# Kernel optimization log

Measured on AMD Instinct MI355X. Metric: run time of the kernel, lower is better.

The kernel has to match this reference:

```python
import jax, jax.numpy as jnp
import numpy as np
from jax import lax

L, H, NUM_CONVS, KSIZE = 8192, 128, 4, 7
EPS = 1e-5


def _pos_encoding(length, dim, dtype):
    pos = jnp.arange(length, dtype=jnp.float32)[:, None]
    i = jnp.arange(dim, dtype=jnp.float32)[None, :]
    angle = pos / jnp.power(10000.0, (2.0 * jnp.floor(i / 2.0)) / dim)
    pe = jnp.where((jnp.arange(dim) % 2 == 0)[None, :], jnp.sin(angle), jnp.cos(angle))
    return pe.astype(dtype)


def _layer_norm(x):
    mu = jnp.mean(x, axis=-1, keepdims=True)
    var = jnp.mean(jnp.square(x - mu), axis=-1, keepdims=True)
    return (x - mu) * lax.rsqrt(var + EPS)


def _conv1d_same(x, w, b):
    # x: [L, H]; w: [H_out, H_in, K]; b: [H_out]. SAME padding over sequence.
    lhs = x.T[None]  # [1, H, L]
    out = lax.conv_general_dilated(lhs, w, window_strides=(1,), padding='SAME',
                                   dimension_numbers=('NCH', 'OIH', 'NCH'))
    return (out[0] + b[:, None]).T  # [L, H]


def setup_inputs() -> dict:
    key = jax.random.key(0)
    ks = jax.random.split(key, 12)
    s = 0.02
    return {
        'x': jax.random.normal(ks[0], (L, H), jnp.float32),
        'conv_w': jax.random.normal(ks[1], (NUM_CONVS, H, H, KSIZE), jnp.float32) * s,
        'conv_b': jax.random.normal(ks[2], (NUM_CONVS, H), jnp.float32) * s,
        'Wq': jax.random.normal(ks[3], (H, H), jnp.float32) * s,
        'bq': jax.random.normal(ks[4], (H,), jnp.float32) * s,
        'Wk': jax.random.normal(ks[5], (H, H), jnp.float32) * s,
        'bk': jax.random.normal(ks[6], (H,), jnp.float32) * s,
        'Wv': jax.random.normal(ks[7], (H, H), jnp.float32) * s,
        'bv': jax.random.normal(ks[8], (H,), jnp.float32) * s,
        'Wff': jax.random.normal(ks[9], (H, H), jnp.float32) * s,
        'bff': jax.random.normal(ks[10], (H,), jnp.float32) * s,
    }


def reference(x, conv_w, conv_b, Wq, bq, Wk, bk, Wv, bv, Wff, bff):
    h = x + _pos_encoding(x.shape[0], x.shape[1], x.dtype)
    # conv stack: LN -> conv -> residual, repeated num_convs times
    for i in range(NUM_CONVS):
        residual = h
        h = _conv1d_same(_layer_norm(h), conv_w[i], conv_b[i]) + residual
    # self-attention (single-head as written in the source)
    residual = h
    n = _layer_norm(h)
    q = n @ Wq.T + bq
    k = n @ Wk.T + bk
    v = n @ Wv.T + bv
    scale = 1.0 / jnp.sqrt(jnp.asarray(H, h.dtype))
    attn = jax.nn.softmax((q @ k.T) * scale, axis=-1)  # [L, L]
    h = attn @ v + residual
    # feed-forward
    residual = h
    h = jax.nn.relu(_layer_norm(h) @ Wff.T + bff) + residual
    return h
```

## Files before the change

### kernel.cpp

```cpp
#include <hip/hip_runtime.h>

#define LL 8192
#define HH 128

typedef __attribute__((ext_vector_type(8))) short short8v;
typedef __attribute__((ext_vector_type(4))) short short4v;
typedef __attribute__((ext_vector_type(4))) float f32x4;
typedef __attribute__((ext_vector_type(16))) float f32x16;

__device__ inline short f2bf(float f) {
    union { float f; unsigned u; } x; x.f = f;
    unsigned r = (x.u + 0x7fffu + ((x.u >> 16) & 1u)) >> 16;
    return (short)r;
}
__device__ inline float bf2f(short s) {
    union { unsigned u; float f; } x; x.u = ((unsigned)(unsigned short)s) << 16;
    return x.f;
}

__device__ inline void plane32swap(unsigned& a, unsigned& b) {
#if defined(__has_builtin)
#if __has_builtin(__builtin_amdgcn_permlane32_swap)
    typedef unsigned u2v __attribute__((ext_vector_type(2)));
    u2v r = __builtin_amdgcn_permlane32_swap(a, b, false, false);
    a = r[0]; b = r[1];
    return;
#endif
#endif
    asm volatile("v_permlane32_swap_b32 %0, %1" : "+v"(a), "+v"(b));
}

__device__ inline short* sAp(short* base, int row, int col) {
    int byte = (row << 8) + (col << 1);
    byte ^= (row & 7) << 4;
    return (short*)((char*)base + byte);
}

__device__ inline short8v ln_pack8(const float* rowF, int l15) {
    const float4 a = *(const float4*)&rowF[l15 * 8];
    const float4 b = *(const float4*)&rowF[l15 * 8 + 4];
    float s  = (a.x + a.y) + (a.z + a.w) + (b.x + b.y) + (b.z + b.w);
    float s2 = a.x * a.x + a.y * a.y + a.z * a.z + a.w * a.w
             + b.x * b.x + b.y * b.y + b.z * b.z + b.w * b.w;
#pragma unroll
    for (int off = 1; off <= 8; off <<= 1) {
        s  += __shfl_xor(s,  off, 64);
        s2 += __shfl_xor(s2, off, 64);
    }
    float mu = s * (1.f / 128.f);
    float var = s2 * (1.f / 128.f) - mu * mu;
    float rstd = rsqrtf(var + 1e-5f);
    short8v r;
    r[0] = f2bf((a.x - mu) * rstd);
    r[1] = f2bf((a.y - mu) * rstd);
    r[2] = f2bf((a.z - mu) * rstd);
    r[3] = f2bf((a.w - mu) * rstd);
    r[4] = f2bf((b.x - mu) * rstd);
    r[5] = f2bf((b.y - mu) * rstd);
    r[6] = f2bf((b.z - mu) * rstd);
    r[7] = f2bf((b.w - mu) * rstd);
    return r;
}

__global__ __launch_bounds__(256) void repack_all(const float* __restrict__ x,
                                                  const float* __restrict__ w,
                                                  const float* __restrict__ Wq,
                                                  const float* __restrict__ Wk,
                                                  const float* __restrict__ Wv,
                                                  const float* __restrict__ bq,
                                                  const float* __restrict__ bk,
                                                  const float* __restrict__ bv,
                                                  const float* __restrict__ Wff,
                                                  short* __restrict__ wkb,
                                                  short* __restrict__ wqkvb,
                                                  float* __restrict__ b3,
                                                  short* __restrict__ wffb,
                                                  float* __restrict__ h0) {
    const float qs = 0.08838834764831845f;
    int idx = blockIdx.x * 256 + threadIdx.x;
    if (idx < 458752) {
        int k = idx % 7;
        int t = idx / 7;
        int i = t % HH; t /= HH;
        int o = t % HH;
        int lay = t / HH;
        wkb[((lay * 7 + k) * HH + o) * HH + i] = f2bf(w[idx]);
    } else {
        int j = idx - 458752;
        if (j < 49152) {
            int t = j >> 14, r = j & 16383;
            float v = (t == 0) ? Wq[r] * qs : (t == 1) ? Wk[r] : Wv[r];
            wqkvb[j] = f2bf(v);
        } else if (j < 49536) {
            int jj = j - 49152;
            b3[jj] = (jj < 128) ? bq[jj] * qs : (jj < 256) ? bk[jj - 128] : bv[jj - 256];
        } else if (j < 65920) {
            int jj = j - 49536;
            wffb[jj] = f2bf(Wff[jj]);
        } else {
            int p = j - 65920;
            if (p < 262144) {
                int g = p >> 5, c4 = (p & 31) << 2;
                float4 val = *(const float4*)&x[g * HH + c4];
                float fg = (float)g;
#pragma unroll
                for (int h = 0; h < 2; h++) {
                    int i0 = c4 + h * 2;
                    float e = (float)i0 / 128.f;
                    float ang = fg / powf(10000.f, e);
                    ((float*)&val)[h * 2]     += sinf(ang);
                    ((float*)&val)[h * 2 + 1] += cosf(ang);
                }
                *(float4*)&h0[g * HH + c4] = val;
            }
        }
    }
}

__global__ __launch_bounds__(256, 4) void conv_layer_kernel(const float* __restrict__ hin,
                                                            const short* __restrict__ wkb,
                                                            const float* __restrict__ conv_b,
                                                            float* __restrict__ hout,
                                                            int lay) {
    __shared__ float sF[22][132];
    __shared__ short sA[22 * 128];
    int tid = threadIdx.x;
    int w = tid >> 6, lane = tid & 63;
    int l15 = lane & 15, quad = lane >> 4;
    int m0 = (blockIdx.x >> 1) * 16;
    int c0w = (blockIdx.x & 1) * 64 + w * 16;

    for (int idx = tid; idx < 22 * 32; idx += 256) {
        int r = idx >> 5, c4 = (idx & 31) << 2;
        int g = m0 - 3 + r;
        float4 val = make_float4(0.f, 0.f, 0.f, 0.f);
        if (g >= 0 && g < LL) val = *(const float4*)&hin[g * HH + c4];
        *(float4*)&sF[r][c4] = val;
    }
    __syncthreads();
#pragma unroll
    for (int rr = 0; rr < 2; rr++) {
        int row = rr * 16 + w * 4 + quad;
        if (row < 22)
            *(short8v*)sAp(sA, row, l15 * 8) = ln_pack8(&sF[row][0], l15);
    }
    __syncthreads();
    f32x4 accA = (f32x4)(0.f), accB = (f32x4)(0.f);
    const short* wl = wkb + lay * 7 * HH * HH;
    for (int k = 0; k < 7; k++) {
        const short* b0 = wl + (k * HH + c0w + l15) * HH;
#pragma unroll
        for (int ks = 0; ks < 4; ks++) {
            short8v bf = *(const short8v*)&b0[ks * 32 + quad * 8];
            short8v af = *(const short8v*)sAp(sA, l15 + k, ks * 32 + quad * 8);
            if (ks & 1) accB = __builtin_amdgcn_mfma_f32_16x16x32_bf16(af, bf, accB, 0, 0, 0);
            else        accA = __builtin_amdgcn_mfma_f32_16x16x32_bf16(af, bf, accA, 0, 0, 0);
        }
    }
    float bb = conv_b[lay * HH + c0w + l15];
#pragma unroll
    for (int r = 0; r < 4; r++) {
        int row = quad * 4 + r;
        hout[(m0 + row) * HH + c0w + l15] =
            sF[3 + row][c0w + l15] + accA[r] + accB[r] + bb;
    }
}

__global__ __launch_bounds__(256, 2) void conv_qkv_kernel(const float* __restrict__ hin,
                                                          const short* __restrict__ wkb,
                                                          const float* __restrict__ conv_b,
                                                          const short* __restrict__ wqkvb,
                                                          const float* __restrict__ b3,
                                                          float* __restrict__ hB,
                                                          short* __restrict__ qb,
                                                          short* __restrict__ kb,
                                                          short* __restrict__ vt) {
    __shared__ float sF[22][132];
    __shared__ short sA[22 * 128];
    __shared__ short sT[4][32][17];
    int tid = threadIdx.x;
    int w = tid >> 6, lane = tid & 63;
    int l15 = lane & 15, quad = lane >> 4;
    int m0 = blockIdx.x * 16;
    int c0 = w * 32;

    for (int idx = tid; idx < 22 * 32; idx += 256) {
        int r = idx >> 5, c4 = (idx & 31) << 2;
        int g = m0 - 3 + r;
        float4 val = make_float4(0.f, 0.f, 0.f, 0.f);
        if (g >= 0 && g < LL) val = *(const float4*)&hin[g * HH + c4];
        *(float4*)&sF[r][c4] = val;
    }
    __syncthreads();
#pragma unroll
    for (int rr = 0; rr < 2; rr++) {
        int row = rr * 16 + w * 4 + quad;
        if (row < 22)
            *(short8v*)sAp(sA, row, l15 * 8) = ln_pack8(&sF[row][0], l15);
    }
    __syncthreads();
    f32x4 a0 = (f32x4)(0.f), a1 = (f32x4)(0.f);
    const short* wl = wkb + 3 * 7 * HH * HH;
    for (int k = 0; k < 7; k++) {
        const short* b0 = wl + (k * HH + c0 + l15) * HH;
        const short* b1 = b0 + 16 * HH;
#pragma unroll
        for (int ks = 0; ks < 4; ks++) {
            short8v bf0 = *(const short8v*)&b0[ks * 32 + quad * 8];
            short8v bf1 = *(const short8v*)&b1[ks * 32 + quad * 8];
            short8v af = *(const short8v*)sAp(sA, l15 + k, ks * 32 + quad * 8);
            a0 = __builtin_amdgcn_mfma_f32_16x16x32_bf16(af, bf0, a0, 0, 0, 0);
            a1 = __builtin_amdgcn_mfma_f32_16x16x32_bf16(af, bf1, a1, 0, 0, 0);
        }
    }
    float bb0 = conv_b[3 * HH + c0 + l15], bb1 = conv_b[3 * HH + c0 + 16 + l15];
#pragma unroll
    for (int r = 0; r < 4; r++) {
        int row = quad * 4 + r;
        float v0 = sF[3 + row][c0 + l15]      + a0[r] + bb0;
        float v1 = sF[3 + row][c0 + 16 + l15] + a1[r] + bb1;
        sF[3 + row][c0 + l15]      = v0;
        sF[3 + row][c0 + 16 + l15] = v1;
        hB[(m0 + row) * HH + c0 + l15]      = v0;
        hB[(m0 + row) * HH + c0 + 16 + l15] = v1;
    }
    __syncthreads();
    {
        int row = w * 4 + quad;
        *(short8v*)sAp(sA, row, l15 * 8) = ln_pack8(&sF[3 + row][0], l15);
    }
    __syncthreads();
    short8v af4[4];
#pragma unroll
    for (int ks = 0; ks < 4; ks++)
        af4[ks] = *(const short8v*)sAp(sA, l15, ks * 32 + quad * 8);

    for (int t = 0; t < 3; t++) {
        f32x4 acc0 = (f32x4)(0.f), acc1 = (f32x4)(0.f);
        const short* b0 = wqkvb + (t * 128 + c0 + l15) * HH;
        const short* b1 = b0 + 16 * HH;
#pragma unroll
        for (int ks = 0; ks < 4; ks++) {
            short8v bf0 = *(const short8v*)&b0[ks * 32 + quad * 8];
            short8v bf1 = *(const short8v*)&b1[ks * 32 + quad * 8];
            acc0 = __builtin_amdgcn_mfma_f32_16x16x32_bf16(af4[ks], bf0, acc0, 0, 0, 0);
            acc1 = __builtin_amdgcn_mfma_f32_16x16x32_bf16(af4[ks], bf1, acc1, 0, 0, 0);
        }
        float qb0 = b3[t * 128 + c0 + l15], qb1 = b3[t * 128 + c0 + 16 + l15];
        if (t < 2) {
            short* o = (t == 0) ? qb : kb;
#pragma unroll
            for (int r = 0; r < 4; r++) {
                int lr = m0 + quad * 4 + r;
                o[lr * HH + c0 + l15]      = f2bf(acc0[r] + qb0);
                o[lr * HH + c0 + 16 + l15] = f2bf(acc1[r] + qb1);
            }
        } else {
#pragma unroll
            for (int r = 0; r < 4; r++) {
                sT[w][l15][quad * 4 + r]      = f2bf(acc0[r] + qb0);
                sT[w][16 + l15][quad * 4 + r] = f2bf(acc1[r] + qb1);
            }
            asm volatile("s_waitcnt lgkmcnt(0)" ::: "memory");
#pragma unroll
            for (int cc = 0; cc < 8; cc++) {
                int col = cc * 4 + quad;
                vt[(c0 + col) * LL + m0 + l15] = sT[w][col][l15];
            }
        }
    }
}

#define FBN 64

__global__ __launch_bounds__(256, 2) void flash_mfma_kernel(const short* __restrict__ qs,
                                                            const short* __restrict__ ksrc,
                                                            const short* __restrict__ vsrc,
                                                            short* __restrict__ PO,
                                                            float* __restrict__ Pl,
                                                            int segrows) {
    __shared__ short sK[2 * 16 * 64 * 8];
    __shared__ short sV[2 * 16 * 64 * 8];

    const int tid = threadIdx.x;
    const int w = tid >> 6, lane = tid & 63;
    const int l31 = lane & 31, hi = lane >> 5;
    const int m0 = blockIdx.x * 128;
    const int seg = blockIdx.y;
    const int jbeg = seg * segrows;
    const int nchunk = segrows >> 6;
    const int qrow = m0 + w * 32 + l31;

    short8v qf[8];
#pragma unroll
    for (int ks = 0; ks < 8; ks++)
        qf[ks] = *(const short8v*)&qs[qrow * HH + ks * 16 + hi * 8];

    float l_r = 0.f;
    f32x16 o_acc[4];
#pragma unroll
    for (int dt = 0; dt < 4; dt++) o_acc[dt] = (f32x16)(0.f);

    short8v kr[4], vr[4];
#pragma unroll
    for (int r = 0; r < 4; r++) {
        int s = w + 4 * r;
        kr[r] = *(const short8v*)&ksrc[(jbeg + (s >> 3) * 32 + l31) * HH + (s & 7) * 16 + hi * 8];
        vr[r] = *(const short8v*)&vsrc[((s >> 2) * 32 + l31) * LL + jbeg + (s & 3) * 16 + hi * 8];
    }
#pragma unroll
    for (int r = 0; r < 4; r++) {
        int s = w + 4 * r;
        *(short8v*)&sK[(s * 64 + lane) * 8] = kr[r];
        *(short8v*)&sV[(s * 64 + lane) * 8] = vr[r];
    }
    if (nchunk > 1) {
        const int j1 = jbeg + FBN;
#pragma unroll
        for (int r = 0; r < 4; r++) {
            int s = w + 4 * r;
            kr[r] = *(const short8v*)&ksrc[(j1 + (s >> 3) * 32 + l31) * HH + (s & 7) * 16 + hi * 8];
            vr[r] = *(const short8v*)&vsrc[((s >> 2) * 32 + l31) * LL + j1 + (s & 3) * 16 + hi * 8];
        }
    }
    __syncthreads();

    int cur = 0;
    for (int c = 0; c < nchunk; c++) {
        const int kb_ = cur * 8192;
        f32x16 s0 = (f32x16)(0.f), s1 = (f32x16)(0.f);
#pragma unroll
        for (int ks = 0; ks < 8; ks++) {
            short8v kf0 = *(const short8v*)&sK[kb_ + ((ks) * 64 + lane) * 8];
            short8v kf1 = *(const short8v*)&sK[kb_ + ((8 + ks) * 64 + lane) * 8];
            s0 = __builtin_amdgcn_mfma_f32_32x32x16_bf16(kf0, qf[ks], s0, 0, 0, 0);
            s1 = __builtin_amdgcn_mfma_f32_32x32x16_bf16(kf1, qf[ks], s1, 0, 0, 0);
        }
        if (c + 1 < nchunk) {
            const int nb = (cur ^ 1) * 8192;
#pragma unroll
            for (int r = 0; r < 4; r++) {
                int s = w + 4 * r;
                *(short8v*)&sK[nb + (s * 64 + lane) * 8] = kr[r];
                *(short8v*)&sV[nb + (s * 64 + lane) * 8] = vr[r];
            }
            if (c + 2 < nchunk) {
                const int j2 = jbeg + (c + 2) * FBN;
#pragma unroll
                for (int r = 0; r < 4; r++) {
                    int s = w + 4 * r;
                    kr[r] = *(const short8v*)&ksrc[(j2 + (s >> 3) * 32 + l31) * HH + (s & 7) * 16 + hi * 8];
                    vr[r] = *(const short8v*)&vsrc[((s >> 2) * 32 + l31) * LL + j2 + (s & 3) * 16 + hi * 8];
                }
            }
        }
        short8v pfrag[4];
#pragma unroll
        for (int nt = 0; nt < 2; nt++) {
            const f32x16& sa = nt ? s1 : s0;
            unsigned pw[8];
#pragma unroll
            for (int m = 0; m < 8; m++) {
                float p0 = __expf(fminf(sa[2 * m], 30.f));
                float p1 = __expf(fminf(sa[2 * m + 1], 30.f));
                l_r += p0 + p1;
                union { float f; unsigned u; } u0, u1;
                u0.f = p0; u1.f = p1;
                pw[m] = (u0.u >> 16) | (u1.u & 0xffff0000u);
            }
            plane32swap(pw[0], pw[2]);
            plane32swap(pw[1], pw[3]);
            plane32swap(pw[4], pw[6]);
            plane32swap(pw[5], pw[7]);
            union { unsigned u[4]; short8v v; } fa, fb;
            fa.u[0] = pw[0]; fa.u[1] = pw[1]; fa.u[2] = pw[2]; fa.u[3] = pw[3];
            fb.u[0] = pw[4]; fb.u[1] = pw[5]; fb.u[2] = pw[6]; fb.u[3] = pw[7];
            pfrag[nt * 2]     = fa.v;
            pfrag[nt * 2 + 1] = fb.v;
        }
#pragma unroll
        for (int ks = 0; ks < 4; ks++)
#pragma unroll
            for (int dt = 0; dt < 4; dt++) {
                short8v vf = *(const short8v*)&sV[kb_ + ((dt * 4 + ks) * 64 + lane) * 8];
                o_acc[dt] = __builtin_amdgcn_mfma_f32_32x32x16_bf16(pfrag[ks], vf, o_acc[dt], 0, 0, 0);
            }
        __syncthreads();
        cur ^= 1;
    }
    float lsum = l_r + __shfl_xor(l_r, 32, 64);
    if (hi == 0)
        Pl[seg * LL + qrow] = lsum;
#pragma unroll
    for (int dt = 0; dt < 4; dt++)
#pragma unroll
        for (int i = 0; i < 16; i++) {
            int qr = (i & 3) + 8 * (i >> 2) + 4 * hi;
            PO[(size_t)seg * LL * HH + (size_t)(m0 + w * 32 + qr) * HH + dt * 32 + l31] =
                f2bf(o_acc[dt][i]);
        }
}

__global__ __launch_bounds__(256) void ff_kernel(const float* __restrict__ hin,
                                                 const short* __restrict__ PO,
                                                 const float* __restrict__ Pl,
                                                 const short* __restrict__ wffb,
                                                 const float* __restrict__ bff,
                                                 float* __restrict__ out,
                                                 int nsplit) {
    __shared__ float sF[16][132];
    __shared__ short sA[16 * 128];
    __shared__ float sLi[16];
    int tid = threadIdx.x;
    int w = tid >> 6, lane = tid & 63;
    int l15 = lane & 15, quad = lane >> 4;
    int m0 = blockIdx.x * 16;

    if (tid < 16) {
        float s = 0.f;
        for (int seg = 0; seg < nsplit; seg++) s += Pl[seg * LL + m0 + tid];
        sLi[tid] = 1.f / s;
    }
    __syncthreads();
    for (int idx = tid; idx < 16 * 32; idx += 256) {
        int r = idx >> 5, c4 = (idx & 31) << 2;
        float4 hv = *(const float4*)&hin[(m0 + r) * HH + c4];
        float s0 = 0.f, s1 = 0.f, s2 = 0.f, s3 = 0.f;
        for (int seg = 0; seg < nsplit; seg++) {
            short4v pv = *(const short4v*)&PO[(size_t)seg * LL * HH + (m0 + r) * HH + c4];
            s0 += bf2f(pv[0]); s1 += bf2f(pv[1]); s2 += bf2f(pv[2]); s3 += bf2f(pv[3]);
        }
        float li = sLi[r];
        *(float4*)&sF[r][c4] = make_float4(hv.x + s0 * li, hv.y + s1 * li,
                                           hv.z + s2 * li, hv.w + s3 * li);
    }
    __syncthreads();
    {
        int row = w * 4 + quad;
        *(short8v*)sAp(sA, row, l15 * 8) = ln_pack8(&sF[row][0], l15);
    }
    __syncthreads();
    int c0 = w * 32;
    f32x4 acc0 = (f32x4)(0.f), acc1 = (f32x4)(0.f);
    const short* b0 = wffb + (c0 + l15) * HH;
    const short* b1 = b0 + 16 * HH;
#pragma unroll
    for (int ks = 0; ks < 4; ks++) {
        short8v af = *(const short8v*)sAp(sA, l15, ks * 32 + quad * 8);
        short8v bf0 = *(const short8v*)&b0[ks * 32 + quad * 8];
        short8v bf1 = *(const short8v*)&b1[ks * 32 + quad * 8];
        acc0 = __builtin_amdgcn_mfma_f32_16x16x32_bf16(af, bf0, acc0, 0, 0, 0);
        acc1 = __builtin_amdgcn_mfma_f32_16x16x32_bf16(af, bf1, acc1, 0, 0, 0);
    }
    float bb0 = bff[c0 + l15], bb1 = bff[c0 + 16 + l15];
#pragma unroll
    for (int r = 0; r < 4; r++) {
        int lr = quad * 4 + r;
        out[(m0 + lr) * HH + c0 + l15]      = fmaxf(acc0[r] + bb0, 0.f) + sF[lr][c0 + l15];
        out[(m0 + lr) * HH + c0 + 16 + l15] = fmaxf(acc1[r] + bb1, 0.f) + sF[lr][c0 + 16 + l15];
    }
}

extern "C" void kernel_launch(void* const* d_in, const int* in_sizes, int n_in,
                              void* d_out, int out_size, void* d_ws, size_t ws_size,
                              hipStream_t stream) {
    const float* x      = (const float*)d_in[0];
    const float* conv_w = (const float*)d_in[1];
    const float* conv_b = (const float*)d_in[2];
    const float* Wq = (const float*)d_in[3];
    const float* bq = (const float*)d_in[4];
    const float* Wk = (const float*)d_in[5];
    const float* bk = (const float*)d_in[6];
    const float* Wv = (const float*)d_in[7];
    const float* bv = (const float*)d_in[8];
    const float* Wff = (const float*)d_in[9];
    const float* bff = (const float*)d_in[10];
    float* out = (float*)d_out;

    char* ws = (char*)d_ws;
    const size_t MB = 1u << 20;
    float* hB   = (float*)(ws);
    short* qb   = (short*)(ws + 4 * MB);
    short* kb   = (short*)(ws + 6 * MB);
    short* vt   = (short*)(ws + 8 * MB);
    float* Pl   = (float*)(ws + 10 * MB);
    short* wffb = (short*)(ws + 10 * MB + 524288);
    short* PO   = (short*)(ws + 10 * MB + 524288 + 32768);
    short* wkb   = (short*)(ws + 16 * MB);
    short* wqkvb = (short*)(ws + 17 * MB);
    float* b3    = (float*)(ws + 17 * MB + 131072);
    float* h0    = (float*)(ws + 18 * MB);
    float* h13   = (float*)(ws + 22 * MB);
    float* h2    = h0;

    const int nsplit = 8;
    const int segrows = LL / nsplit;

    repack_all<<<3074, 256, 0, stream>>>(x, conv_w, Wq, Wk, Wv, bq, bk, bv, Wff,
                                         wkb, wqkvb, b3, wffb, h0);
    conv_layer_kernel<<<LL / 16 * 2, 256, 0, stream>>>(h0,  wkb, conv_b, h13, 0);
    conv_layer_kernel<<<LL / 16 * 2, 256, 0, stream>>>(h13, wkb, conv_b, h2,  1);
    conv_layer_kernel<<<LL / 16 * 2, 256, 0, stream>>>(h2,  wkb, conv_b, h13, 2);
    conv_qkv_kernel<<<LL / 16, 256, 0, stream>>>(h13, wkb, conv_b, wqkvb, b3,
                                                 hB, qb, kb, vt);
    flash_mfma_kernel<<<dim3(LL / 128, nsplit), 256, 0, stream>>>(qb, kb, vt, PO, Pl, segrows);
    ff_kernel<<<LL / 16, 256, 0, stream>>>(hB, PO, Pl, wffb, bff, out, nsplit);
}
```

Measured before the change: 211.6 us.

## Single-buffer flash LDS, exp2 softmax, setprio, and XCD-aware block remapping

The flash kernel goes from double-buffered to single-buffered LDS for K/V, using register prefetch with two barriers per chunk. It also wraps the MFMA phases in s_setprio. Softmax now uses a native exp2 with log2e folded into the Q scale, and drops the clamp at 30. P packing uses a perm instruction. Block indices in the conv, qkv, flash and ff kernels are remapped so neighbouring tiles land on the same XCD for L2 locality. The exp clamp removal could overflow for large logits, and the extra barrier reduces overlap.

```diff
diff --git a/kernel.cpp b/kernel.cpp
--- a/kernel.cpp
+++ b/kernel.cpp
@@ -16,6 +16,27 @@
 __device__ inline float bf2f(short s) {
     union { unsigned u; float f; } x; x.u = ((unsigned)(unsigned short)s) << 16;
     return x.f;
+}
+
+__device__ inline float fexp2(float x) {
+#if defined(__has_builtin)
+#if __has_builtin(__builtin_amdgcn_exp2f)
+    return __builtin_amdgcn_exp2f(x);
+#else
+    return __expf(x * 0.6931471805599453f);
+#endif
+#else
+    return __expf(x * 0.6931471805599453f);
+#endif
+}
+
+__device__ inline unsigned pack_hi16(unsigned hi, unsigned lo) {
+#if defined(__has_builtin)
+#if __has_builtin(__builtin_amdgcn_perm)
+    return __builtin_amdgcn_perm(hi, lo, 0x07060302u);
+#endif
+#endif
+    return (lo >> 16) | (hi & 0xffff0000u);
 }
 
 __device__ inline void plane32swap(unsigned& a, unsigned& b) {
@@ -76,7 +97,7 @@
                                                   float* __restrict__ b3,
                                                   short* __restrict__ wffb,
                                                   float* __restrict__ h0) {
-    const float qs = 0.08838834764831845f;
+    const float qs = 0.08838834764831845f * 1.4426950408889634f;
     int idx = blockIdx.x * 256 + threadIdx.x;
     if (idx < 458752) {
         int k = idx % 7;
@@ -127,8 +148,9 @@
     int tid = threadIdx.x;
     int w = tid >> 6, lane = tid & 63;
     int l15 = lane & 15, quad = lane >> 4;
-    int m0 = (blockIdx.x >> 1) * 16;
-    int c0w = (blockIdx.x & 1) * 64 + w * 16;
+    int wg = blockIdx.x;
+    int m0 = ((wg & 7) * 64 + (wg >> 4)) * 16;
+    int c0w = (((wg >> 3) & 1)) * 64 + w * 16;
 
     for (int idx = tid; idx < 22 * 32; idx += 256) {
         int r = idx >> 5, c4 = (idx & 31) << 2;
@@ -181,7 +203,8 @@
     int tid = threadIdx.x;
     int w = tid >> 6, lane = tid & 63;
     int l15 = lane & 15, quad = lane >> 4;
-    int m0 = blockIdx.x * 16;
+    int wg = blockIdx.x;
+    int m0 = ((wg & 7) * 64 + (wg >> 3)) * 16;
     int c0 = w * 32;
 
     for (int idx = tid; idx < 22 * 32; idx += 256) {
@@ -279,14 +302,14 @@
                                                             short* __restrict__ PO,
                                                             float* __restrict__ Pl,
                                                             int segrows) {
-    __shared__ short sK[2 * 16 * 64 * 8];
-    __shared__ short sV[2 * 16 * 64 * 8];
+    __shared__ short sK[16 * 64 * 8];
+    __shared__ short sV[16 * 64 * 8];
 
     const int tid = threadIdx.x;
     const int w = tid >> 6, lane = tid & 63;
     const int l31 = lane & 31, hi = lane >> 5;
-    const int m0 = blockIdx.x * 128;
-    const int seg = blockIdx.y;
+    const int seg = blockIdx.x & 7;
+    const int m0 = (blockIdx.x >> 3) * 128;
     const int jbeg = seg * segrows;
     const int nchunk = segrows >> 6;
     const int qrow = m0 + w * 32 + l31;
@@ -308,52 +331,35 @@
         kr[r] = *(const short8v*)&ksrc[(jbeg + (s >> 3) * 32 + l31) * HH + (s & 7) * 16 + hi * 8];
         vr[r] = *(const short8v*)&vsrc[((s >> 2) * 32 + l31) * LL + jbeg + (s & 3) * 16 + hi * 8];
     }
-#pragma unroll
-    for (int r = 0; r < 4; r++) {
-        int s = w + 4 * r;
-        *(short8v*)&sK[(s * 64 + lane) * 8] = kr[r];
-        *(short8v*)&sV[(s * 64 + lane) * 8] = vr[r];
-    }
-    if (nchunk > 1) {
-        const int j1 = jbeg + FBN;
+
+    for (int c = 0; c < nchunk; c++) {
+        __syncthreads();
 #pragma unroll
         for (int r = 0; r < 4; r++) {
             int s = w + 4 * r;
-            kr[r] = *(const short8v*)&ksrc[(j1 + (s >> 3) * 32 + l31) * HH + (s & 7) * 16 + hi * 8];
-            vr[r] = *(const short8v*)&vsrc[((s >> 2) * 32 + l31) * LL + j1 + (s & 3) * 16 + hi * 8];
-        }
-    }
-    __syncthreads();
-
-    int cur = 0;
-    for (int c = 0; c < nchunk; c++) {
-        const int kb_ = cur * 8192;
+            *(short8v*)&sK[(s * 64 + lane) * 8] = kr[r];
+            *(short8v*)&sV[(s * 64 + lane) * 8] = vr[r];
+        }
+        __syncthreads();
+        if (c + 1 < nchunk) {
+            const int j1 = jbeg + (c + 1) * FBN;
+#pragma unroll
+            for (int r = 0; r < 4; r++) {
+                int s = w + 4 * r;
+                kr[r] = *(const short8v*)&ksrc[(j1 + (s >> 3) * 32 + l31) * HH + (s & 7) * 16 + hi * 8];
+                vr[r] = *(const short8v*)&vsrc[((s >> 2) * 32 + l31) * LL + j1 + (s & 3) * 16 + hi * 8];
+            }
+        }
         f32x16 s0 = (f32x16)(0.f), s1 = (f32x16)(0.f);
+        __builtin_amdgcn_s_setprio(1);
 #pragma unroll
         for (int ks = 0; ks < 8; ks++) {
-            short8v kf0 = *(const short8v*)&sK[kb_ + ((ks) * 64 + lane) * 8];
-            short8v kf1 = *(const short8v*)&sK[kb_ + ((8 + ks) * 64 + lane) * 8];
+            short8v kf0 = *(const short8v*)&sK[((ks) * 64 + lane) * 8];
+            short8v kf1 = *(const short8v*)&sK[((8 + ks) * 64 + lane) * 8];
             s0 = __builtin_amdgcn_mfma_f32_32x32x16_bf16(kf0, qf[ks], s0, 0, 0, 0);
             s1 = __builtin_amdgcn_mfma_f32_32x32x16_bf16(kf1, qf[ks], s1, 0, 0, 0);
         }
-        if (c + 1 < nchunk) {
-            const int nb = (cur ^ 1) * 8192;
-#pragma unroll
-            for (int r = 0; r < 4; r++) {
-                int s = w + 4 * r;
-                *(short8v*)&sK[nb + (s * 64 + lane) * 8] = kr[r];
-                *(short8v*)&sV[nb + (s * 64 + lane) * 8] = vr[r];
-            }
-            if (c + 2 < nchunk) {
-                const int j2 = jbeg + (c + 2) * FBN;
-#pragma unroll
-                for (int r = 0; r < 4; r++) {
-                    int s = w + 4 * r;
-                    kr[r] = *(const short8v*)&ksrc[(j2 + (s >> 3) * 32 + l31) * HH + (s & 7) * 16 + hi * 8];
-                    vr[r] = *(const short8v*)&vsrc[((s >> 2) * 32 + l31) * LL + j2 + (s & 3) * 16 + hi * 8];
-                }
-            }
-        }
+        __builtin_amdgcn_s_setprio(0);
         short8v pfrag[4];
 #pragma unroll
         for (int nt = 0; nt < 2; nt++) {
@@ -361,12 +367,12 @@
             unsigned pw[8];
 #pragma unroll
             for (int m = 0; m < 8; m++) {
-                float p0 = __expf(fminf(sa[2 * m], 30.f));
-                float p1 = __expf(fminf(sa[2 * m + 1], 30.f));
+                float p0 = fexp2(sa[2 * m]);
+                float p1 = fexp2(sa[2 * m + 1]);
                 l_r += p0 + p1;
                 union { float f; unsigned u; } u0, u1;
                 u0.f = p0; u1.f = p1;
-                pw[m] = (u0.u >> 16) | (u1.u & 0xffff0000u);
+                pw[m] = pack_hi16(u1.u, u0.u);
             }
             plane32swap(pw[0], pw[2]);
             plane32swap(pw[1], pw[3]);
@@ -378,15 +384,15 @@
             pfrag[nt * 2]     = fa.v;
             pfrag[nt * 2 + 1] = fb.v;
         }
+        __builtin_amdgcn_s_setprio(1);
 #pragma unroll
         for (int ks = 0; ks < 4; ks++)
 #pragma unroll
             for (int dt = 0; dt < 4; dt++) {
-                short8v vf = *(const short8v*)&sV[kb_ + ((dt * 4 + ks) * 64 + lane) * 8];
+                short8v vf = *(const short8v*)&sV[((dt * 4 + ks) * 64 + lane) * 8];
                 o_acc[dt] = __builtin_amdgcn_mfma_f32_32x32x16_bf16(pfrag[ks], vf, o_acc[dt], 0, 0, 0);
             }
-        __syncthreads();
-        cur ^= 1;
+        __builtin_amdgcn_s_setprio(0);
     }
     float lsum = l_r + __shfl_xor(l_r, 32, 64);
     if (hi == 0)
@@ -414,7 +420,8 @@
     int tid = threadIdx.x;
     int w = tid >> 6, lane = tid & 63;
     int l15 = lane & 15, quad = lane >> 4;
-    int m0 = blockIdx.x * 16;
+    int wg = blockIdx.x;
+    int m0 = ((wg & 7) * 64 + (wg >> 3)) * 16;
 
     if (tid < 16) {
         float s = 0.f;
@@ -503,6 +510,6 @@
     conv_layer_kernel<<<LL / 16 * 2, 256, 0, stream>>>(h2,  wkb, conv_b, h13, 2);
     conv_qkv_kernel<<<LL / 16, 256, 0, stream>>>(h13, wkb, conv_b, wqkvb, b3,
                                                  hB, qb, kb, vt);
-    flash_mfma_kernel<<<dim3(LL / 128, nsplit), 256, 0, stream>>>(qb, kb, vt, PO, Pl, segrows);
+    flash_mfma_kernel<<<LL / 128 * nsplit, 256, 0, stream>>>(qb, kb, vt, PO, Pl, segrows);
     ff_kernel<<<LL / 16, 256, 0, stream>>>(hB, PO, Pl, wffb, bff, out, nsplit);
 }
```

After: 205.8 us. 2.7% less time.
